# Kernel optimization log

Measured on AMD Instinct MI355X. Metric: run time of the kernel, lower is better.

The kernel has to match this reference:

```python
import jax, jax.numpy as jnp
import numpy as np

N_NODES = 50000
N_EDGES = 800000
D = 128
N_LAYERS = 4
NUM_GRAPHS = 128
BN_EPS = 1e-5


def setup_inputs() -> dict:
    key = jax.random.key(0)
    ks = jax.random.split(key, 10)
    x = jax.random.normal(ks[0], (N_NODES, D), dtype=jnp.float32)
    edge_index = jax.random.randint(ks[1], (2, N_EDGES), 0, N_NODES, dtype=jnp.int64)
    batch = jnp.sort(jax.random.randint(ks[2], (N_NODES,), 0, NUM_GRAPHS, dtype=jnp.int64))
    # GINConv MLP params: Linear(D->D), ReLU, Linear(D->D); stacked over layers.
    scale = 1.0 / np.sqrt(D)
    W1 = jax.random.normal(ks[3], (N_LAYERS, D, D), dtype=jnp.float32) * scale
    b1 = jnp.zeros((N_LAYERS, D), dtype=jnp.float32)
    W2 = jax.random.normal(ks[4], (N_LAYERS, D, D), dtype=jnp.float32) * scale
    b2 = jnp.zeros((N_LAYERS, D), dtype=jnp.float32)
    eps = jnp.zeros((N_LAYERS,), dtype=jnp.float32)  # train_eps=True, init 0
    bn_gamma = jnp.ones((N_LAYERS - 1, D), dtype=jnp.float32)
    bn_beta = jnp.zeros((N_LAYERS - 1, D), dtype=jnp.float32)
    return {"x": x, "edge_index": edge_index, "batch": batch,
            "W1": W1, "b1": b1, "W2": W2, "b2": b2, "eps": eps,
            "bn_gamma": bn_gamma, "bn_beta": bn_beta}


def reference(x, edge_index, batch, W1, b1, W2, b2, eps, bn_gamma, bn_beta):
    src, dst = edge_index[0], edge_index[1]
    h = x
    for i in range(N_LAYERS):
        # GINConv: MLP((1+eps)*x_i + sum_{j->i} x_j)
        agg = jax.ops.segment_sum(h[src], dst, num_segments=N_NODES)  # [N, D]
        z = (1.0 + eps[i]) * h + agg
        z = jnp.maximum(z @ W1[i] + b1[i], 0.0) @ W2[i] + b2[i]
        if i < N_LAYERS - 1:
            # BatchNorm1d (training-mode batch statistics) + ReLU
            mu = jnp.mean(z, axis=0)
            var = jnp.var(z, axis=0)
            z = (z - mu) * jax.lax.rsqrt(var + BN_EPS) * bn_gamma[i] + bn_beta[i]
            z = jnp.maximum(z, 0.0)
        h = z
    # global_add_pool
    return jax.ops.segment_sum(h, batch, num_segments=NUM_GRAPHS)  # [G, D]
```

## Files before the change

kernel.cpp:

```cpp
#include <hip/hip_runtime.h>

#define N_NODES 50000
#define N_EDGES 800000
#define D 128
#define NUM_GRAPHS 128

typedef __attribute__((ext_vector_type(8)))  short bfrag8;
typedef __attribute__((ext_vector_type(16))) float f32x16;

__device__ __forceinline__ float4 f4zero() { return make_float4(0.f, 0.f, 0.f, 0.f); }

__device__ __forceinline__ unsigned short f2bf(float f) {
    unsigned u = __float_as_uint(f);
    unsigned r = (u + 0x7fffu + ((u >> 16) & 1u)) >> 16;
    return (unsigned short)r;
}
__device__ __forceinline__ float bf2f(unsigned short b) {
    return __uint_as_float(((unsigned)b) << 16);
}
__device__ __forceinline__ float4 bf2f4(ushort4 u) {
    return make_float4(bf2f(u.x), bf2f(u.y), bf2f(u.z), bf2f(u.w));
}
__device__ __forceinline__ float4 bnrelu(float4 v, float4 a, float4 b) {
    v.x = fmaxf(a.x * v.x + b.x, 0.f);
    v.y = fmaxf(a.y * v.y + b.y, 0.f);
    v.z = fmaxf(a.z * v.z + b.z, 0.f);
    v.w = fmaxf(a.w * v.w + b.w, 0.f);
    return v;
}
__device__ __forceinline__ void acc4(float4& a, float4 u) {
    a.x += u.x; a.y += u.y; a.z += u.z; a.w += u.w;
}

__global__ __launch_bounds__(256) void prep_kernel(
    const float* __restrict__ W1, const float* __restrict__ W2,
    const float* __restrict__ x, short* __restrict__ Wt,
    ushort4* __restrict__ Hb, int* __restrict__ deg, float* __restrict__ stats)
{
    int b = blockIdx.x, t = threadIdx.x;
    if (b < 512) {
        int idx = b * 256 + t;
        int m = idx >> 14, rem = idx & 16383;
        int k = rem >> 7, n = rem & 127;
        const float* W = (m < 4) ? (W1 + (size_t)m * 16384)
                                 : (W2 + (size_t)(m - 4) * 16384);
        Wt[(size_t)m * 16384 + n * 128 + k] = (short)f2bf(W[k * 128 + n]);
    } else if (b < 6762) {
        int i = (b - 512) * 256 + t;
        float4 v = ((const float4*)x)[i];
        Hb[i] = make_ushort4(f2bf(v.x), f2bf(v.y), f2bf(v.z), f2bf(v.w));
    } else if (b < 6958) {
        int i = (b - 6762) * 256 + t;
        if (i < N_NODES) deg[i] = 0;
    } else {
        int i = (b - 6958) * 256 + t;
        stats[i] = 0.f;
    }
}

__global__ __launch_bounds__(256) void hist_kernel(
    const int* __restrict__ dst, int* __restrict__ deg,
    int* __restrict__ edge_pos)
{
    int e = blockIdx.x * 256 + threadIdx.x;
    if (e < N_EDGES) edge_pos[e] = atomicAdd(&deg[dst[e]], 1);
}

__global__ __launch_bounds__(256) void scan_block_kernel(
    const int* __restrict__ deg, int* __restrict__ row_ptr,
    int* __restrict__ blockSum)
{
    __shared__ int wsum[4];
    int t = threadIdx.x, b = blockIdx.x;
    int i = b * 256 + t;
    int v = (i < N_NODES) ? deg[i] : 0;
    int lane = t & 63, wid = t >> 6;
    #pragma unroll
    for (int off = 1; off < 64; off <<= 1) {
        int u = __shfl_up(v, off, 64);
        if (lane >= off) v += u;
    }
    if (lane == 63) wsum[wid] = v;
    __syncthreads();
    int add = 0;
    for (int w = 0; w < wid; ++w) add += wsum[w];
    v += add;
    if (i < N_NODES) row_ptr[i + 1] = v;
    if (t == 255) blockSum[b] = v;
}

__global__ __launch_bounds__(256) void scan_fixup_kernel(
    const int* __restrict__ blockSum, int* __restrict__ row_ptr, int nb)
{
    __shared__ int wsum[4];
    __shared__ int sbuf[256];
    int t = threadIdx.x, b = blockIdx.x;
    int v = (t < nb) ? blockSum[t] : 0;
    int lane = t & 63, wid = t >> 6;
    #pragma unroll
    for (int off = 1; off < 64; off <<= 1) {
        int u = __shfl_up(v, off, 64);
        if (lane >= off) v += u;
    }
    if (lane == 63) wsum[wid] = v;
    __syncthreads();
    int add = 0;
    for (int w = 0; w < wid; ++w) add += wsum[w];
    sbuf[t] = v + add;
    __syncthreads();
    if (b == 0 && t == 0) row_ptr[0] = 0;
    if (b > 0) {
        int off = sbuf[b - 1];
        int i = b * 256 + t;
        if (i < N_NODES) row_ptr[i + 1] += off;
    }
}

__global__ __launch_bounds__(256) void fill_kernel(
    const int* __restrict__ src, const int* __restrict__ dst,
    const int* __restrict__ row_ptr, const int* __restrict__ edge_pos,
    int* __restrict__ csr_src)
{
    int e = blockIdx.x * 256 + threadIdx.x;
    if (e >= N_EDGES) return;
    csr_src[row_ptr[dst[e]] + edge_pos[e]] = src[e];
}

__global__ __launch_bounds__(256) void gather_kernel(
    const ushort4* __restrict__ H, const int* __restrict__ row_ptr,
    const int* __restrict__ csr_src,
    const float* __restrict__ stats,
    const float* __restrict__ gamma, const float* __restrict__ beta,
    const float* __restrict__ epsp,
    ushort4* __restrict__ A)
{
    int node = blockIdx.x * 8 + (threadIdx.x >> 5);
    if (node >= N_NODES) return;
    int lane = threadIdx.x & 31;
    const bool bn = (stats != nullptr);
    float4 sa = make_float4(1.f, 1.f, 1.f, 1.f);
    float4 sb = f4zero();
    if (bn) {
        const float invN = 1.0f / (float)N_NODES;
        float m0 = stats[lane * 4 + 0] * invN, m1 = stats[lane * 4 + 1] * invN;
        float m2 = stats[lane * 4 + 2] * invN, m3 = stats[lane * 4 + 3] * invN;
        sa.x = gamma[lane * 4 + 0] * rsqrtf(stats[128 + lane * 4 + 0] * invN - m0 * m0 + 1e-5f);
        sa.y = gamma[lane * 4 + 1] * rsqrtf(stats[128 + lane * 4 + 1] * invN - m1 * m1 + 1e-5f);
        sa.z = gamma[lane * 4 + 2] * rsqrtf(stats[128 + lane * 4 + 2] * invN - m2 * m2 + 1e-5f);
        sa.w = gamma[lane * 4 + 3] * rsqrtf(stats[128 + lane * 4 + 3] * invN - m3 * m3 + 1e-5f);
        sb.x = beta[lane * 4 + 0] - m0 * sa.x;
        sb.y = beta[lane * 4 + 1] - m1 * sa.y;
        sb.z = beta[lane * 4 + 2] - m2 * sa.z;
        sb.w = beta[lane * 4 + 3] - m3 * sa.w;
    }
    float eps1 = 1.0f + *epsp;
    int beg = row_ptr[node], end = row_ptr[node + 1];

    float4 v = bf2f4(H[node * 32 + lane]);
    if (bn) v = bnrelu(v, sa, sb);
    float4 acc = make_float4(eps1 * v.x, eps1 * v.y, eps1 * v.z, eps1 * v.w);

    for (int base = beg; base < end; base += 32) {
        int idx = (base + lane < end) ? csr_src[base + lane] : 0;
        int cnt = min(32, end - base);
        int j = 0;
        for (; j + 8 <= cnt; j += 8) {
            int s0 = __shfl(idx, j + 0, 32), s1 = __shfl(idx, j + 1, 32);
            int s2 = __shfl(idx, j + 2, 32), s3 = __shfl(idx, j + 3, 32);
            int s4 = __shfl(idx, j + 4, 32), s5 = __shfl(idx, j + 5, 32);
            int s6 = __shfl(idx, j + 6, 32), s7 = __shfl(idx, j + 7, 32);
            float4 u0 = bf2f4(H[s0 * 32 + lane]);
            float4 u1 = bf2f4(H[s1 * 32 + lane]);
            float4 u2 = bf2f4(H[s2 * 32 + lane]);
            float4 u3 = bf2f4(H[s3 * 32 + lane]);
            float4 u4 = bf2f4(H[s4 * 32 + lane]);
            float4 u5 = bf2f4(H[s5 * 32 + lane]);
            float4 u6 = bf2f4(H[s6 * 32 + lane]);
            float4 u7 = bf2f4(H[s7 * 32 + lane]);
            if (bn) {
                u0 = bnrelu(u0, sa, sb); u1 = bnrelu(u1, sa, sb);
                u2 = bnrelu(u2, sa, sb); u3 = bnrelu(u3, sa, sb);
                u4 = bnrelu(u4, sa, sb); u5 = bnrelu(u5, sa, sb);
                u6 = bnrelu(u6, sa, sb); u7 = bnrelu(u7, sa, sb);
            }
            acc4(acc, u0); acc4(acc, u1); acc4(acc, u2); acc4(acc, u3);
            acc4(acc, u4); acc4(acc, u5); acc4(acc, u6); acc4(acc, u7);
        }
        for (; j < cnt; ++j) {
            int s = __shfl(idx, j, 32);
            float4 u = bf2f4(H[s * 32 + lane]);
            if (bn) u = bnrelu(u, sa, sb);
            acc4(acc, u);
        }
    }
    A[node * 32 + lane] = make_ushort4(f2bf(acc.x), f2bf(acc.y),
                                       f2bf(acc.z), f2bf(acc.w));
}

__global__ __launch_bounds__(256, 3) void mlp_fused_kernel(
    const ushort* __restrict__ A,
    const short* __restrict__ Wt1,
    const short* __restrict__ Wt2,
    const float* __restrict__ bias1,
    const float* __restrict__ bias2,
    ushort* __restrict__ Hout,
    float* __restrict__ statsSum,
    float* __restrict__ statsSq,
    int M)
{
    __shared__ __align__(16) short Wlds[128 * 128];
    __shared__ __align__(16) short zlds[2][32 * 128];
    __shared__ float ssum[128];
    __shared__ float ssq[128];

    const int tid  = threadIdx.x;
    const int wv   = tid >> 6;
    const int lane = tid & 63;
    const int half = lane >> 5;
    const int ln   = lane & 31;
    const int rg   = wv & 1;
    const int ch   = wv >> 1;
    const int row0 = blockIdx.x * 64 + rg * 32;
    const bool doStats = (statsSum != nullptr);
    if (doStats && tid < 128) { ssum[tid] = 0.f; ssq[tid] = 0.f; }

    short* zw = &zlds[rg][0];

    {
        const int4* Wg = (const int4*)Wt1;
        int4* Wl = (int4*)Wlds;
        #pragma unroll
        for (int i = 0; i < 8; ++i) {
            int id = i * 256 + tid;
            int n = id >> 4, c = id & 15;
            Wl[n * 16 + (c ^ (n & 15))] = Wg[id];
        }
    }
    __syncthreads();

    {
        f32x16 acc[2];
        #pragma unroll
        for (int ci = 0; ci < 2; ++ci)
            #pragma unroll
            for (int r = 0; r < 16; ++r) acc[ci][r] = 0.f;

        bfrag8 af[8];
        int rowc = min(row0 + ln, M - 1);
        const ushort* ap = A + (size_t)rowc * 128 + half * 8;
        #pragma unroll
        for (int kk = 0; kk < 8; ++kk)
            af[kk] = *(const bfrag8*)(ap + kk * 16);

        #pragma unroll
        for (int kk = 0; kk < 8; ++kk) {
            #pragma unroll
            for (int ci = 0; ci < 2; ++ci) {
                int n = (ch * 2 + ci) * 32 + ln;
                int c = kk * 2 + half;
                bfrag8 bf = *(const bfrag8*)(Wlds + n * 128 + ((c ^ (n & 15)) << 3));
                acc[ci] = __builtin_amdgcn_mfma_f32_32x32x16_bf16(
                    af[kk], bf, acc[ci], 0, 0, 0);
            }
        }
        #pragma unroll
        for (int ci = 0; ci < 2; ++ci) {
            int col = (ch * 2 + ci) * 32 + ln;
            int cc = col >> 3, co = col & 7;
            float bv = bias1[col];
            #pragma unroll
            for (int r = 0; r < 16; ++r) {
                int rloc = (r & 3) + 8 * (r >> 2) + 4 * half;
                float v = fmaxf(acc[ci][r] + bv, 0.f);
                zw[rloc * 128 + ((cc ^ (rloc & 15)) << 3) + co] = (short)f2bf(v);
            }
        }
    }
    __syncthreads();

    bfrag8 af2[8];
    #pragma unroll
    for (int kk = 0; kk < 8; ++kk) {
        int c = kk * 2 + half;
        af2[kk] = *(const bfrag8*)(zw + ln * 128 + ((c ^ (ln & 15)) << 3));
    }
    {
        const int4* Wg = (const int4*)Wt2;
        int4* Wl = (int4*)Wlds;
        #pragma unroll
        for (int i = 0; i < 8; ++i) {
            int id = i * 256 + tid;
            int n = id >> 4, c = id & 15;
            Wl[n * 16 + (c ^ (n & 15))] = Wg[id];
        }
    }
    __syncthreads();

    {
        f32x16 acc[2];
        #pragma unroll
        for (int ci = 0; ci < 2; ++ci)
            #pragma unroll
            for (int r = 0; r < 16; ++r) acc[ci][r] = 0.f;

        #pragma unroll
        for (int kk = 0; kk < 8; ++kk) {
            #pragma unroll
            for (int ci = 0; ci < 2; ++ci) {
                int n = (ch * 2 + ci) * 32 + ln;
                int c = kk * 2 + half;
                bfrag8 bf = *(const bfrag8*)(Wlds + n * 128 + ((c ^ (n & 15)) << 3));
                acc[ci] = __builtin_amdgcn_mfma_f32_32x32x16_bf16(
                    af2[kk], bf, acc[ci], 0, 0, 0);
            }
        }
        #pragma unroll
        for (int ci = 0; ci < 2; ++ci) {
            int col = (ch * 2 + ci) * 32 + ln;
            int cc = col >> 3, co = col & 7;
            float bv = bias2[col];
            float s = 0.f, sq = 0.f;
            #pragma unroll
            for (int r = 0; r < 16; ++r) {
                int rloc = (r & 3) + 8 * (r >> 2) + 4 * half;
                float v = acc[ci][r] + bv;
                zw[rloc * 128 + ((cc ^ (rloc & 15)) << 3) + co] = (short)f2bf(v);
                if (row0 + rloc < M) { s += v; sq += v * v; }
            }
            if (doStats) {
                s  += __shfl_xor(s, 32);
                sq += __shfl_xor(sq, 32);
                if (half == 0) {
                    atomicAdd(&ssum[col], s);
                    atomicAdd(&ssq[col], sq);
                }
            }
        }
    }
    __syncthreads();

    {
        int4* Ho = (int4*)Hout;
        #pragma unroll
        for (int i = 0; i < 4; ++i) {
            int id = i * 256 + tid;
            int r = id >> 4, c = id & 15;
            int rl = r & 31;
            int grow = blockIdx.x * 64 + r;
            if (grow < M)
                Ho[(size_t)grow * 16 + c] =
                    ((const int4*)&zlds[r >> 5][0])[rl * 16 + (c ^ (rl & 15))];
        }
    }
    if (doStats && tid < 128) {
        atomicAdd(&statsSum[tid], ssum[tid]);
        atomicAdd(&statsSq[tid],  ssq[tid]);
    }
}

__global__ __launch_bounds__(256) void pool_kernel(
    const ushort4* __restrict__ H, const int* __restrict__ batch,
    float* __restrict__ out)
{
    int c4 = threadIdx.x & 31;
    int nl = threadIdx.x >> 5;
    int node0 = blockIdx.x * 256;
    float4 acc = f4zero();
    int gcur = -1;
    for (int i = nl; i < 256; i += 8) {
        int n = node0 + i;
        if (n >= N_NODES) break;
        int g = batch[n];
        if (g != gcur) {
            if (gcur >= 0) {
                float* o = out + gcur * D + c4 * 4;
                atomicAdd(o + 0, acc.x); atomicAdd(o + 1, acc.y);
                atomicAdd(o + 2, acc.z); atomicAdd(o + 3, acc.w);
            }
            gcur = g;
            acc = f4zero();
        }
        float4 v = bf2f4(H[n * 32 + c4]);
        acc4(acc, v);
    }
    if (gcur >= 0) {
        float* o = out + gcur * D + c4 * 4;
        atomicAdd(o + 0, acc.x); atomicAdd(o + 1, acc.y);
        atomicAdd(o + 2, acc.z); atomicAdd(o + 3, acc.w);
    }
}

extern "C" void kernel_launch(void* const* d_in, const int* in_sizes, int n_in,
                              void* d_out, int out_size, void* d_ws, size_t ws_size,
                              hipStream_t stream)
{
    const float* x     = (const float*)d_in[0];
    const int*   ei    = (const int*)d_in[1];
    const int*   batch = (const int*)d_in[2];
    const float* W1    = (const float*)d_in[3];
    const float* b1    = (const float*)d_in[4];
    const float* W2    = (const float*)d_in[5];
    const float* b2    = (const float*)d_in[6];
    const float* eps   = (const float*)d_in[7];
    const float* gamma = (const float*)d_in[8];
    const float* beta  = (const float*)d_in[9];
    float* out = (float*)d_out;

    unsigned short* Hb  = (unsigned short*)d_ws;
    unsigned short* Abf = Hb + (size_t)N_NODES * D;
    float* stats    = (float*)(Abf + (size_t)N_NODES * D);
    int*   deg      = (int*)(stats + 3 * 256);
    int*   row_ptr  = deg + N_NODES;
    int*   blockSum = row_ptr + N_NODES + 1;
    int*   edge_pos = blockSum + 256;
    int*   csr_src  = edge_pos + N_EDGES;
    short* Wt       = (short*)(csr_src + N_EDGES);

    const int* src = ei;
    const int* dst = ei + N_EDGES;

    const int edgeBlocks   = (N_EDGES + 255) / 256;
    const int scanBlocks   = (N_NODES + 255) / 256;
    const int gatherBlocks = (N_NODES + 7) / 8;
    const int gemmBlocks   = (N_NODES + 63) / 64;

    prep_kernel<<<6961, 256, 0, stream>>>(W1, W2, x, Wt, (ushort4*)Hb,
                                          deg, stats);
    hist_kernel<<<edgeBlocks, 256, 0, stream>>>(dst, deg, edge_pos);
    scan_block_kernel<<<scanBlocks, 256, 0, stream>>>(deg, row_ptr, blockSum);
    scan_fixup_kernel<<<scanBlocks, 256, 0, stream>>>(blockSum, row_ptr, scanBlocks);
    fill_kernel<<<edgeBlocks, 256, 0, stream>>>(src, dst, row_ptr, edge_pos, csr_src);

    for (int layer = 0; layer < 4; ++layer) {
        const bool bn = (layer < 3);
        const float* statPrev = (layer == 0) ? nullptr : stats + (layer - 1) * 256;
        int gl = (layer > 0) ? layer - 1 : 0;
        gather_kernel<<<gatherBlocks, 256, 0, stream>>>(
            (const ushort4*)Hb, row_ptr, csr_src, statPrev,
            gamma + (size_t)gl * D, beta + (size_t)gl * D,
            eps + layer, (ushort4*)Abf);
        mlp_fused_kernel<<<gemmBlocks, 256, 0, stream>>>(
            Abf, Wt + (size_t)layer * 16384, Wt + (size_t)(4 + layer) * 16384,
            b1 + (size_t)layer * D, b2 + (size_t)layer * D, Hb,
            bn ? stats + layer * 256 : nullptr,
            bn ? stats + layer * 256 + 128 : nullptr, N_NODES);
    }

    hipMemsetAsync(out, 0, (size_t)NUM_GRAPHS * D * sizeof(float), stream);
    pool_kernel<<<scanBlocks, 256, 0, stream>>>(
        (const ushort4*)Hb, batch, out);
}
```

Before: 421.6 us.

## Apply BatchNorm in a separate pass and gather with 16-byte loads

BatchNorm+ReLU moves out of the gather into a dedicated in-place kernel that normalizes H once per layer, so the gather no longer repeats the affine and ReLU per edge. The gather now uses 16 lanes per node with uint4 (8 bf16) loads instead of 32 lanes with ushort4, which widens each memory request and packs more nodes per block. The cost is an extra full read and write of H per layer and an extra kernel launch, plus an added bf16 rounding after normalization. The bounds check on node in the gather is removed, which is safe only because N_NODES is divisible by 16.

New measurement: 411.6 us. -2.4%, faster.

```diff
diff --git a/kernel.cpp b/kernel.cpp
--- a/kernel.cpp
+++ b/kernel.cpp
@@ -21,15 +21,18 @@
 __device__ __forceinline__ float4 bf2f4(ushort4 u) {
     return make_float4(bf2f(u.x), bf2f(u.y), bf2f(u.z), bf2f(u.w));
 }
-__device__ __forceinline__ float4 bnrelu(float4 v, float4 a, float4 b) {
-    v.x = fmaxf(a.x * v.x + b.x, 0.f);
-    v.y = fmaxf(a.y * v.y + b.y, 0.f);
-    v.z = fmaxf(a.z * v.z + b.z, 0.f);
-    v.w = fmaxf(a.w * v.w + b.w, 0.f);
-    return v;
-}
 __device__ __forceinline__ void acc4(float4& a, float4 u) {
     a.x += u.x; a.y += u.y; a.z += u.z; a.w += u.w;
+}
+__device__ __forceinline__ void acc8(float* a, uint4 r) {
+    a[0] += __uint_as_float(r.x << 16);
+    a[1] += __uint_as_float(r.x & 0xffff0000u);
+    a[2] += __uint_as_float(r.y << 16);
+    a[3] += __uint_as_float(r.y & 0xffff0000u);
+    a[4] += __uint_as_float(r.z << 16);
+    a[5] += __uint_as_float(r.z & 0xffff0000u);
+    a[6] += __uint_as_float(r.w << 16);
+    a[7] += __uint_as_float(r.w & 0xffff0000u);
 }
 
 __global__ __launch_bounds__(256) void prep_kernel(
@@ -126,75 +129,101 @@
     csr_src[row_ptr[dst[e]] + edge_pos[e]] = src[e];
 }
 
+__global__ __launch_bounds__(256) void bnapply_kernel(
+    uint4* __restrict__ H, const float* __restrict__ stats,
+    const float* __restrict__ gamma, const float* __restrict__ beta)
+{
+    __shared__ float sa[128], sb[128];
+    int tid = threadIdx.x;
+    if (tid < 128) {
+        const float invN = 1.0f / (float)N_NODES;
+        float m = stats[tid] * invN;
+        float a = gamma[tid] * rsqrtf(stats[128 + tid] * invN - m * m + 1e-5f);
+        sa[tid] = a;
+        sb[tid] = beta[tid] - m * a;
+    }
+    __syncthreads();
+    int id = blockIdx.x * 256 + tid;
+    int c0 = (id & 15) * 8;
+    uint4 u = H[id];
+    float lo, hi;
+    lo = fmaxf(sa[c0 + 0] * __uint_as_float(u.x << 16)          + sb[c0 + 0], 0.f);
+    hi = fmaxf(sa[c0 + 1] * __uint_as_float(u.x & 0xffff0000u) + sb[c0 + 1], 0.f);
+    u.x = (unsigned)f2bf(lo) | ((unsigned)f2bf(hi) << 16);
+    lo = fmaxf(sa[c0 + 2] * __uint_as_float(u.y << 16)          + sb[c0 + 2], 0.f);
+    hi = fmaxf(sa[c0 + 3] * __uint_as_float(u.y & 0xffff0000u) + sb[c0 + 3], 0.f);
+    u.y = (unsigned)f2bf(lo) | ((unsigned)f2bf(hi) << 16);
+    lo = fmaxf(sa[c0 + 4] * __uint_as_float(u.z << 16)          + sb[c0 + 4], 0.f);
+    hi = fmaxf(sa[c0 + 5] * __uint_as_float(u.z & 0xffff0000u) + sb[c0 + 5], 0.f);
+    u.z = (unsigned)f2bf(lo) | ((unsigned)f2bf(hi) << 16);
+    lo = fmaxf(sa[c0 + 6] * __uint_as_float(u.w << 16)          + sb[c0 + 6], 0.f);
+    hi = fmaxf(sa[c0 + 7] * __uint_as_float(u.w & 0xffff0000u) + sb[c0 + 7], 0.f);
+    u.w = (unsigned)f2bf(lo) | ((unsigned)f2bf(hi) << 16);
+    H[id] = u;
+}
+
 __global__ __launch_bounds__(256) void gather_kernel(
-    const ushort4* __restrict__ H, const int* __restrict__ row_ptr,
-    const int* __restrict__ csr_src,
-    const float* __restrict__ stats,
-    const float* __restrict__ gamma, const float* __restrict__ beta,
-    const float* __restrict__ epsp,
-    ushort4* __restrict__ A)
-{
-    int node = blockIdx.x * 8 + (threadIdx.x >> 5);
-    if (node >= N_NODES) return;
-    int lane = threadIdx.x & 31;
-    const bool bn = (stats != nullptr);
-    float4 sa = make_float4(1.f, 1.f, 1.f, 1.f);
-    float4 sb = f4zero();
-    if (bn) {
-        const float invN = 1.0f / (float)N_NODES;
-        float m0 = stats[lane * 4 + 0] * invN, m1 = stats[lane * 4 + 1] * invN;
-        float m2 = stats[lane * 4 + 2] * invN, m3 = stats[lane * 4 + 3] * invN;
-        sa.x = gamma[lane * 4 + 0] * rsqrtf(stats[128 + lane * 4 + 0] * invN - m0 * m0 + 1e-5f);
-        sa.y = gamma[lane * 4 + 1] * rsqrtf(stats[128 + lane * 4 + 1] * invN - m1 * m1 + 1e-5f);
-        sa.z = gamma[lane * 4 + 2] * rsqrtf(stats[128 + lane * 4 + 2] * invN - m2 * m2 + 1e-5f);
-        sa.w = gamma[lane * 4 + 3] * rsqrtf(stats[128 + lane * 4 + 3] * invN - m3 * m3 + 1e-5f);
-        sb.x = beta[lane * 4 + 0] - m0 * sa.x;
-        sb.y = beta[lane * 4 + 1] - m1 * sa.y;
-        sb.z = beta[lane * 4 + 2] - m2 * sa.z;
-        sb.w = beta[lane * 4 + 3] - m3 * sa.w;
-    }
+    const uint4* __restrict__ H, const int* __restrict__ row_ptr,
+    const int* __restrict__ csr_src, const float* __restrict__ epsp,
+    uint4* __restrict__ A)
+{
+    int node = blockIdx.x * 16 + (threadIdx.x >> 4);
+    int lane = threadIdx.x & 15;
     float eps1 = 1.0f + *epsp;
     int beg = row_ptr[node], end = row_ptr[node + 1];
 
-    float4 v = bf2f4(H[node * 32 + lane]);
-    if (bn) v = bnrelu(v, sa, sb);
-    float4 acc = make_float4(eps1 * v.x, eps1 * v.y, eps1 * v.z, eps1 * v.w);
-
-    for (int base = beg; base < end; base += 32) {
+    uint4 hv = H[node * 16 + lane];
+    float acc[8];
+    acc[0] = eps1 * __uint_as_float(hv.x << 16);
+    acc[1] = eps1 * __uint_as_float(hv.x & 0xffff0000u);
+    acc[2] = eps1 * __uint_as_float(hv.y << 16);
+    acc[3] = eps1 * __uint_as_float(hv.y & 0xffff0000u);
+    acc[4] = eps1 * __uint_as_float(hv.z << 16);
+    acc[5] = eps1 * __uint_as_float(hv.z & 0xffff0000u);
+    acc[6] = eps1 * __uint_as_float(hv.w << 16);
+    acc[7] = eps1 * __uint_as_float(hv.w & 0xffff0000u);
+
+    for (int base = beg; base < end; base += 16) {
         int idx = (base + lane < end) ? csr_src[base + lane] : 0;
-        int cnt = min(32, end - base);
+        int cnt = min(16, end - base);
         int j = 0;
         for (; j + 8 <= cnt; j += 8) {
-            int s0 = __shfl(idx, j + 0, 32), s1 = __shfl(idx, j + 1, 32);
-            int s2 = __shfl(idx, j + 2, 32), s3 = __shfl(idx, j + 3, 32);
-            int s4 = __shfl(idx, j + 4, 32), s5 = __shfl(idx, j + 5, 32);
-            int s6 = __shfl(idx, j + 6, 32), s7 = __shfl(idx, j + 7, 32);
-            float4 u0 = bf2f4(H[s0 * 32 + lane]);
-            float4 u1 = bf2f4(H[s1 * 32 + lane]);
-            float4 u2 = bf2f4(H[s2 * 32 + lane]);
-            float4 u3 = bf2f4(H[s3 * 32 + lane]);
-            float4 u4 = bf2f4(H[s4 * 32 + lane]);
-            float4 u5 = bf2f4(H[s5 * 32 + lane]);
-            float4 u6 = bf2f4(H[s6 * 32 + lane]);
-            float4 u7 = bf2f4(H[s7 * 32 + lane]);
-            if (bn) {
-                u0 = bnrelu(u0, sa, sb); u1 = bnrelu(u1, sa, sb);
-                u2 = bnrelu(u2, sa, sb); u3 = bnrelu(u3, sa, sb);
-                u4 = bnrelu(u4, sa, sb); u5 = bnrelu(u5, sa, sb);
-                u6 = bnrelu(u6, sa, sb); u7 = bnrelu(u7, sa, sb);
-            }
-            acc4(acc, u0); acc4(acc, u1); acc4(acc, u2); acc4(acc, u3);
-            acc4(acc, u4); acc4(acc, u5); acc4(acc, u6); acc4(acc, u7);
+            int s0 = __shfl(idx, j + 0, 16), s1 = __shfl(idx, j + 1, 16);
+            int s2 = __shfl(idx, j + 2, 16), s3 = __shfl(idx, j + 3, 16);
+            int s4 = __shfl(idx, j + 4, 16), s5 = __shfl(idx, j + 5, 16);
+            int s6 = __shfl(idx, j + 6, 16), s7 = __shfl(idx, j + 7, 16);
+            uint4 u0 = H[s0 * 16 + lane];
+            uint4 u1 = H[s1 * 16 + lane];
+            uint4 u2 = H[s2 * 16 + lane];
+            uint4 u3 = H[s3 * 16 + lane];
+            uint4 u4 = H[s4 * 16 + lane];
+            uint4 u5 = H[s5 * 16 + lane];
+            uint4 u6 = H[s6 * 16 + lane];
+            uint4 u7 = H[s7 * 16 + lane];
+            acc8(acc, u0); acc8(acc, u1); acc8(acc, u2); acc8(acc, u3);
+            acc8(acc, u4); acc8(acc, u5); acc8(acc, u6); acc8(acc, u7);
+        }
+        for (; j + 4 <= cnt; j += 4) {
+            int s0 = __shfl(idx, j + 0, 16), s1 = __shfl(idx, j + 1, 16);
+            int s2 = __shfl(idx, j + 2, 16), s3 = __shfl(idx, j + 3, 16);
+            uint4 u0 = H[s0 * 16 + lane];
+            uint4 u1 = H[s1 * 16 + lane];
+            uint4 u2 = H[s2 * 16 + lane];
+            uint4 u3 = H[s3 * 16 + lane];
+            acc8(acc, u0); acc8(acc, u1); acc8(acc, u2); acc8(acc, u3);
         }
         for (; j < cnt; ++j) {
-            int s = __shfl(idx, j, 32);
-            float4 u = bf2f4(H[s * 32 + lane]);
-            if (bn) u = bnrelu(u, sa, sb);
-            acc4(acc, u);
-        }
-    }
-    A[node * 32 + lane] = make_ushort4(f2bf(acc.x), f2bf(acc.y),
-                                       f2bf(acc.z), f2bf(acc.w));
+            int s = __shfl(idx, j, 16);
+            uint4 u = H[s * 16 + lane];
+            acc8(acc, u);
+        }
+    }
+    uint4 o;
+    o.x = (unsigned)f2bf(acc[0]) | ((unsigned)f2bf(acc[1]) << 16);
+    o.y = (unsigned)f2bf(acc[2]) | ((unsigned)f2bf(acc[3]) << 16);
+    o.z = (unsigned)f2bf(acc[4]) | ((unsigned)f2bf(acc[5]) << 16);
+    o.w = (unsigned)f2bf(acc[6]) | ((unsigned)f2bf(acc[7]) << 16);
+    A[node * 16 + lane] = o;
 }
 
 __global__ __launch_bounds__(256, 3) void mlp_fused_kernel(
@@ -421,7 +450,8 @@
 
     const int edgeBlocks   = (N_EDGES + 255) / 256;
     const int scanBlocks   = (N_NODES + 255) / 256;
-    const int gatherBlocks = (N_NODES + 7) / 8;
+    const int gatherBlocks = (N_NODES + 15) / 16;
+    const int bnBlocks     = (N_NODES * 16) / 256;
     const int gemmBlocks   = (N_NODES + 63) / 64;
 
     prep_kernel<<<6961, 256, 0, stream>>>(W1, W2, x, Wt, (ushort4*)Hb,
@@ -433,12 +463,13 @@
 
     for (int layer = 0; layer < 4; ++layer) {
         const bool bn = (layer < 3);
-        const float* statPrev = (layer == 0) ? nullptr : stats + (layer - 1) * 256;
-        int gl = (layer > 0) ? layer - 1 : 0;
+        if (layer > 0) {
+            bnapply_kernel<<<bnBlocks, 256, 0, stream>>>(
+                (uint4*)Hb, stats + (size_t)(layer - 1) * 256,
+                gamma + (size_t)(layer - 1) * D, beta + (size_t)(layer - 1) * D);
+        }
         gather_kernel<<<gatherBlocks, 256, 0, stream>>>(
-            (const ushort4*)Hb, row_ptr, csr_src, statPrev,
-            gamma + (size_t)gl * D, beta + (size_t)gl * D,
-            eps + layer, (ushort4*)Abf);
+            (const uint4*)Hb, row_ptr, csr_src, eps + layer, (uint4*)Abf);
         mlp_fused_kernel<<<gemmBlocks, 256, 0, stream>>>(
             Abf, Wt + (size_t)layer * 16384, Wt + (size_t)(4 + layer) * 16384,
             b1 + (size_t)layer * D, b2 + (size_t)layer * D, Hb,
```
